# Performance work log

Measured on AMD Instinct MI355X. Metric: run time of the kernel, lower is better.

## Reference

```python
import jax, jax.numpy as jnp
import numpy as np

B = 2
SP = (480, 360, 32)   # spatial_shape (z, y, x)
GS = (8, 8, 8)        # query_gs_ratio
EP = (40, 15, 16)     # embed_params (pool compress ratio)
H = 8
N = 120000
D = 256
OUT = 20


def _dims(rat):
    return tuple((s + r - 1) // r for s, r in zip(SP, rat))


def sine_pe(coords, d_pos):
    # coords: [M,3] float voxel coords in original grid units; normalized sine PE
    nf = d_pos // 6
    sp = jnp.asarray(SP, jnp.float32)
    cn = coords / sp * (2.0 * jnp.pi)                      # normalize=True
    t = 10000.0 ** (jnp.arange(nf, dtype=jnp.float32) / nf)
    ang = cn[:, :, None] / t                               # [M,3,nf]
    pe = jnp.concatenate([jnp.sin(ang), jnp.cos(ang)], -1).reshape(coords.shape[0], -1)
    return jnp.pad(pe, ((0, 0), (0, d_pos - 6 * nf)))


def setup_inputs() -> dict:
    key = jax.random.key(0)
    ks = jax.random.split(key, 24)
    idx_b = jax.random.randint(ks[0], (N, 1), 0, B)
    idx_z = jax.random.randint(ks[1], (N, 1), 0, SP[0])
    idx_y = jax.random.randint(ks[2], (N, 1), 0, SP[1])
    idx_x = jax.random.randint(ks[3], (N, 1), 0, SP[2])
    indices = jnp.concatenate([idx_b, idx_z, idx_y, idx_x], axis=1).astype(jnp.int32)
    s = D ** -0.5
    p = lambda k, sh: jax.random.normal(k, sh, jnp.float32) * s
    return {
        'features': jax.random.normal(ks[4], (N, D), jnp.float32),
        'W_pool': p(ks[5], (D, D)), 'b_pool': jnp.zeros((D,), jnp.float32),
        'W_emb': p(ks[6], (D, D)), 'b_emb': jnp.zeros((D,), jnp.float32),
        'Wq': p(ks[7], (D, D)), 'bq': jnp.zeros((D,), jnp.float32),
        'Wk': p(ks[8], (D, D)), 'bk': jnp.zeros((D,), jnp.float32),
        'Wv': p(ks[9], (D, D)), 'bv': jnp.zeros((D,), jnp.float32),
        'Wo': p(ks[10], (D, D)), 'bo': jnp.zeros((D,), jnp.float32),
        'ln_g': jnp.ones((D,), jnp.float32), 'ln_b': jnp.zeros((D,), jnp.float32),
        'W_seg': p(ks[11], (D, OUT)), 'b_seg': jnp.zeros((OUT,), jnp.float32),
        'indices': indices,
        'batch_size': B,
    }


def reference(features, W_pool, b_pool, W_emb, b_emb, Wq, bq, Wk, bk, Wv, bv,
              Wo, bo, ln_g, ln_b, W_seg, b_seg, indices, batch_size):
    Zd, Yd, Xd = _dims(GS)
    Gq = Zd * Yd * Xd
    Sq = batch_size * Gq
    Ze, Ye, Xe = _dims(EP)
    Gk = Ze * Ye * Xe
    Sk = batch_size * Gk
    n = features.shape[0]

    # --- query pool branch: linear -> voxel-grid scatter_max ---
    pf = features @ W_pool + b_pool                                    # [N,D]
    dq = indices[:, 1:] // jnp.asarray(GS, jnp.int32)
    seg_q = ((indices[:, 0] * Zd + dq[:, 0]) * Yd + dq[:, 1]) * Xd + dq[:, 2]
    pool_max = jax.ops.segment_max(pf, seg_q, num_segments=Sq)
    cnt_q = jax.ops.segment_sum(jnp.ones((n,), jnp.float32), seg_q, num_segments=Sq)
    mq = cnt_q > 0
    pool_max = jnp.where(mq[:, None], pool_max, 0.0)
    cell = jnp.arange(Sq)
    rem = cell % Gq
    pool_c = jnp.stack([(rem // (Yd * Xd)) * GS[0],
                        ((rem // Xd) % Yd) * GS[1],
                        (rem % Xd) * GS[2]], -1).astype(jnp.float32)   # [Sq,3]

    # --- embedding branch ('pool'): linear -> coarse scatter_max + per-channel argmax coords ---
    ef = features @ W_emb + b_emb                                      # [N,D]
    de = indices[:, 1:] // jnp.asarray(EP, jnp.int32)
    seg_k = ((indices[:, 0] * Ze + de[:, 0]) * Ye + de[:, 1]) * Xe + de[:, 2]
    emb_max = jax.ops.segment_max(ef, seg_k, num_segments=Sk)
    cnt_k = jax.ops.segment_sum(jnp.ones((n,), jnp.float32), seg_k, num_segments=Sk)
    mk = cnt_k > 0
    emb_max = jnp.where(mk[:, None], emb_max, 0.0)
    winner = ef == jnp.where(mk[:, None], emb_max, -jnp.inf)[seg_k]
    idx = jax.ops.segment_max(jnp.where(winner, jnp.arange(n)[:, None], -1), seg_k, num_segments=Sk)
    idx_c = jnp.clip(idx, 0, n - 1)                                    # [Sk,D]
    ec = de.astype(jnp.float32)                                        # [N,3] downsampled coords
    emb_c = ec[idx_c].mean(axis=1) * jnp.asarray(EP, jnp.float32)      # [Sk,3]

    # --- position encoding (pointwise sine PE; per-batch loop in torch is pointwise-equivalent) ---
    pool_max = pool_max + sine_pe(pool_c, D)
    emb_max = emb_max + sine_pe(emb_c, D)

    # --- multi-head cross-attention (Q=pool, K/V=embedding), per-batch via dense grid reshape ---
    q_in = pool_max.reshape(batch_size, Gq, D)
    kv_in = emb_max.reshape(batch_size, Gk, D)
    dh = D // H
    q = (q_in @ Wq + bq).reshape(batch_size, Gq, H, dh)
    k = (kv_in @ Wk + bk).reshape(batch_size, Gk, H, dh)
    v = (kv_in @ Wv + bv).reshape(batch_size, Gk, H, dh)
    scores = jnp.einsum('bqhd,bkhd->bhqk', q, k) / jnp.float32(dh) ** 0.5
    kmask = mk.reshape(batch_size, Gk)
    scores = jnp.where(kmask[:, None, None, :], scores, -1e9)
    attn = jax.nn.softmax(scores, axis=-1)
    o = jnp.einsum('bhqk,bkhd->bqhd', attn, v).reshape(batch_size, Gq, D) @ Wo + bo
    h = q_in + o                                                       # residual + LayerNorm sublayer
    mu = h.mean(-1, keepdims=True)
    var = h.var(-1, keepdims=True)
    h = (h - mu) * jax.lax.rsqrt(var + 1e-5) * ln_g + ln_b
    feats_mhca = h.reshape(Sq, D)

    # --- gather back to voxels via pool_inv, residual, seg head (center-tap of SubMConv3d) ---
    vox = features + feats_mhca[seg_q]
    logits = vox @ W_seg + b_seg
    return logits
```

## Files before the change

kernel.cpp:

```cpp
#include <hip/hip_runtime.h>
#include <math.h>

#define N_PTS 120000
#define D 256
#define BATCH 2
#define NH 8
#define DH 32
#define OUTC 20

#define Zd 60
#define Yd 45
#define Xd 4
#define Gq 10800
#define Sq 21600

#define Ze 12
#define Ye 24
#define Xe 2
#define Gk 576
#define Sk 1152

typedef __bf16 bf16_t;
typedef __attribute__((ext_vector_type(8))) __bf16 bf16x8;
typedef __attribute__((ext_vector_type(4))) __bf16 bf16x4;
typedef __attribute__((ext_vector_type(4))) float f32x4;

__device__ __forceinline__ void glds16(const void* g, void* l) {
    __builtin_amdgcn_global_load_lds(
        (const __attribute__((address_space(1))) unsigned int*)g,
        (__attribute__((address_space(3))) unsigned int*)l,
        16, 0, 0);
}

__global__ __launch_bounds__(256) void k_prep(
    const float* __restrict__ Wp, const float* __restrict__ We,
    const float* __restrict__ Wq, const float* __restrict__ Wk,
    const float* __restrict__ Wv, const float* __restrict__ Wo,
    const float* __restrict__ bp, const float* __restrict__ be,
    const float* __restrict__ bk, const float* __restrict__ bv,
    const float* __restrict__ Wseg, const float* __restrict__ bseg,
    bf16_t* __restrict__ Wpe, bf16_t* __restrict__ Wqt,
    bf16_t* __restrict__ Wkv, bf16_t* __restrict__ Wot,
    bf16_t* __restrict__ Wsegt,
    float* __restrict__ bpe, float* __restrict__ bkv,
    float* __restrict__ bsegp)
{
    int n = blockIdx.x, k = threadIdx.x;
    if (n < 512) {
        const float* S = (n < 256) ? Wp : We;
        int nn = n & 255;
        Wpe[n * 256 + k] = (bf16_t)S[k * 256 + nn];
    } else if (n < 768) {
        int nn = n - 512;
        Wqt[nn * 256 + k] = (bf16_t)Wq[k * 256 + nn];
    } else if (n < 1280) {
        int m2 = n - 768;
        const float* S = (m2 < 256) ? Wk : Wv;
        int nn = m2 & 255;
        Wkv[m2 * 256 + k] = (bf16_t)S[k * 256 + nn];
    } else if (n < 1536) {
        int nn = n - 1280;
        Wot[nn * 256 + k] = (bf16_t)Wo[k * 256 + nn];
    } else if (n == 1536) {
        bpe[k] = bp[k]; bpe[256 + k] = be[k];
        bkv[k] = bk[k]; bkv[256 + k] = bv[k];
        if (k < 32) bsegp[k] = (k < OUTC) ? bseg[k] : 0.f;
    } else {
        int n2 = n - 1537;
        Wsegt[n2 * 256 + k] = (n2 < OUTC) ? (bf16_t)Wseg[k * OUTC + n2] : (bf16_t)0.f;
    }
}

__global__ __launch_bounds__(256) void k_cast(
    const float* __restrict__ in, bf16_t* __restrict__ out)
{
    const size_t total = (size_t)N_PTS * 32;
    const size_t stride = (size_t)gridDim.x * 256;
    for (size_t i = (size_t)blockIdx.x * 256 + threadIdx.x; i < total; i += stride) {
        float4 a = *(const float4*)(in + i * 8);
        float4 b = *(const float4*)(in + i * 8 + 4);
        bf16x8 o;
        o[0] = (bf16_t)a.x; o[1] = (bf16_t)a.y; o[2] = (bf16_t)a.z; o[3] = (bf16_t)a.w;
        o[4] = (bf16_t)b.x; o[5] = (bf16_t)b.y; o[6] = (bf16_t)b.z; o[7] = (bf16_t)b.w;
        *(bf16x8*)(out + i * 8) = o;
    }
}

__global__ __launch_bounds__(256) void k_count(
    const int* __restrict__ indices, int* __restrict__ cnt_q, int* __restrict__ cnt_k,
    int* __restrict__ segq, int* __restrict__ segk)
{
    int i = blockIdx.x * 256 + threadIdx.x;
    if (i >= N_PTS) return;
    const int* id = indices + (size_t)i * 4;
    int b = id[0], z = id[1], y = id[2], x = id[3];
    int sq = ((b * Zd + (z >> 3)) * Yd + (y >> 3)) * Xd + (x >> 3);
    int sk = ((b * Ze + (z / 40)) * Ye + (y / 15)) * Xe + (x >> 4);
    segq[i] = sq; segk[i] = sk;
    atomicAdd(&cnt_q[sq], 1);
    atomicAdd(&cnt_k[sk], 1);
}

__global__ __launch_bounds__(1024) void k_scan(
    const int* __restrict__ cnt, int n, int* __restrict__ offs, int* __restrict__ cursor)
{
    __shared__ int wbase[17];
    __shared__ int carry_s;
    const int t = threadIdx.x, lane = t & 63, w = t >> 6;
    if (t == 0) carry_s = 0;
    __syncthreads();
    for (int base = 0; base < n; base += 1024) {
        int v = (base + t < n) ? cnt[base + t] : 0;
        int incl = v;
        #pragma unroll
        for (int off = 1; off < 64; off <<= 1) {
            int u = __shfl_up(incl, off);
            if (lane >= off) incl += u;
        }
        if (lane == 63) wbase[w + 1] = incl;
        __syncthreads();
        if (t == 0) {
            int s = 0;
            wbase[0] = 0;
            #pragma unroll
            for (int i = 1; i <= 16; ++i) { s += wbase[i]; wbase[i] = s; }
        }
        __syncthreads();
        int excl = incl - v + wbase[w] + carry_s;
        if (base + t < n) { offs[base + t] = excl; cursor[base + t] = excl; }
        __syncthreads();
        if (t == 0) carry_s += wbase[16];
        __syncthreads();
    }
}

__global__ __launch_bounds__(256) void k_place(
    const int* __restrict__ segq, const int* __restrict__ segk,
    int* __restrict__ cur_q, int* __restrict__ cur_k,
    int* __restrict__ ids_q, int* __restrict__ ids_k)
{
    int i = blockIdx.x * 256 + threadIdx.x;
    if (i >= N_PTS) return;
    ids_q[atomicAdd(&cur_q[segq[i]], 1)] = i;
    ids_k[atomicAdd(&cur_k[segk[i]], 1)] = i;
}

__global__ __launch_bounds__(256, 4) void k_gemm_bf(
    const bf16_t* __restrict__ A, int M,
    const bf16_t* __restrict__ Wt, const float* __restrict__ bias,
    bf16_t* __restrict__ outb, int ldo)
{
    __shared__ __align__(16) bf16_t Abuf[128 * 64];
    __shared__ __align__(16) bf16_t Bbuf[128 * 64];

    const int t = threadIdx.x;
    const int wave = t >> 6, lane = t & 63;
    const int wr = wave >> 1, wc = wave & 1;
    const int lrow = lane & 15, quad = lane >> 4;
    const int lr8 = lane >> 3, lc8 = lane & 7;
    const int row0 = blockIdx.y * 128;
    const int ntile = blockIdx.x;

    f32x4 acc[4][4];
    #pragma unroll
    for (int mi = 0; mi < 4; ++mi)
        #pragma unroll
        for (int ni = 0; ni < 4; ++ni)
            acc[mi][ni] = (f32x4){0.f, 0.f, 0.f, 0.f};

    for (int k0 = 0; k0 < 256; k0 += 64) {
        #pragma unroll
        for (int i = 0; i < 4; ++i) {
            int chunk = wave * 4 + i;
            int rowA = row0 + chunk * 8 + lr8;
            if (rowA > M - 1) rowA = M - 1;
            glds16(A + (size_t)rowA * 256 + k0 + lc8 * 8, &Abuf[chunk * 512]);
        }
        #pragma unroll
        for (int i = 0; i < 4; ++i) {
            int chunk = wave * 4 + i;
            glds16(Wt + (size_t)(ntile * 128 + chunk * 8 + lr8) * 256 + k0 + lc8 * 8,
                   &Bbuf[chunk * 512]);
        }
        asm volatile("s_waitcnt vmcnt(0)" ::: "memory");
        __builtin_amdgcn_sched_barrier(0);
        __syncthreads();

        #pragma unroll
        for (int kk = 0; kk < 64; kk += 32) {
            bf16x8 Af[4], Bf[4];
            #pragma unroll
            for (int mi = 0; mi < 4; ++mi)
                Af[mi] = *(const bf16x8*)&Abuf[(wr * 64 + mi * 16 + lrow) * 64 + kk + quad * 8];
            #pragma unroll
            for (int ni = 0; ni < 4; ++ni)
                Bf[ni] = *(const bf16x8*)&Bbuf[(wc * 64 + ni * 16 + lrow) * 64 + kk + quad * 8];
            #pragma unroll
            for (int mi = 0; mi < 4; ++mi)
                #pragma unroll
                for (int ni = 0; ni < 4; ++ni)
                    acc[mi][ni] = __builtin_amdgcn_mfma_f32_16x16x32_bf16(
                        Af[mi], Bf[ni], acc[mi][ni], 0, 0, 0);
        }
        __syncthreads();
    }

    const int colb = ntile * 128 + wc * 64;
    float biasv[4];
    #pragma unroll
    for (int ni = 0; ni < 4; ++ni) biasv[ni] = bias[colb + ni * 16 + lrow];

    #pragma unroll
    for (int mi = 0; mi < 4; ++mi) {
        int lr = wr * 64 + mi * 16 + quad * 4;
        #pragma unroll
        for (int reg = 0; reg < 4; ++reg) {
            int grow = row0 + lr + reg;
            if (grow >= M) continue;
            #pragma unroll
            for (int ni = 0; ni < 4; ++ni) {
                int col = colb + ni * 16 + lrow;
                outb[(size_t)grow * ldo + col] = (bf16_t)(acc[mi][ni][reg] + biasv[ni]);
            }
        }
    }
}

__global__ __launch_bounds__(512, 2) void k_gemm(
    const float* __restrict__ A, int M,
    const bf16_t* __restrict__ Wt, const float* __restrict__ bias,
    int mode, float* __restrict__ outp, int ldo)
{
    __shared__ __align__(16) bf16_t Abuf[128][72];
    __shared__ __align__(16) bf16_t Bbuf[256][72];

    const int t = threadIdx.x;
    const int wave = t >> 6, lane = t & 63;
    const int wr = wave >> 2, wc = wave & 3;
    const int lrow = lane & 15, quad = lane >> 4;
    const int row0 = blockIdx.y * 128;
    const int ntile = blockIdx.x;

    f32x4 acc[4][4];
    #pragma unroll
    for (int mi = 0; mi < 4; ++mi)
        #pragma unroll
        for (int ni = 0; ni < 4; ++ni)
            acc[mi][ni] = (f32x4){0.f, 0.f, 0.f, 0.f};

    for (int k0 = 0; k0 < 256; k0 += 64) {
        #pragma unroll
        for (int i = 0; i < 4; ++i) {
            int c = i * 512 + t;
            int r = c >> 4, c4 = c & 15;
            float4 v = make_float4(0.f, 0.f, 0.f, 0.f);
            if (row0 + r < M)
                v = *(const float4*)(A + (size_t)(row0 + r) * 256 + k0 + c4 * 4);
            bf16x4 bv4;
            bv4[0] = (bf16_t)v.x; bv4[1] = (bf16_t)v.y;
            bv4[2] = (bf16_t)v.z; bv4[3] = (bf16_t)v.w;
            *(bf16x4*)&Abuf[r][c4 * 4] = bv4;
        }
        #pragma unroll
        for (int i = 0; i < 4; ++i) {
            int c = i * 512 + t;
            int r = c >> 3, c8 = c & 7;
            uint4 w = *(const uint4*)(Wt + ((size_t)(ntile * 256 + r)) * 256 + k0 + c8 * 8);
            *(uint4*)&Bbuf[r][c8 * 8] = w;
        }
        __syncthreads();

        #pragma unroll
        for (int kk = 0; kk < 64; kk += 32) {
            bf16x8 Af[4], Bf[4];
            #pragma unroll
            for (int mi = 0; mi < 4; ++mi)
                Af[mi] = *(const bf16x8*)&Abuf[wr * 64 + mi * 16 + lrow][kk + quad * 8];
            #pragma unroll
            for (int ni = 0; ni < 4; ++ni)
                Bf[ni] = *(const bf16x8*)&Bbuf[wc * 64 + ni * 16 + lrow][kk + quad * 8];
            #pragma unroll
            for (int mi = 0; mi < 4; ++mi)
                #pragma unroll
                for (int ni = 0; ni < 4; ++ni)
                    acc[mi][ni] = __builtin_amdgcn_mfma_f32_16x16x32_bf16(
                        Af[mi], Bf[ni], acc[mi][ni], 0, 0, 0);
        }
        __syncthreads();
    }

    const int colb = ntile * 256 + wc * 64;
    float biasv[4];
    #pragma unroll
    for (int ni = 0; ni < 4; ++ni) biasv[ni] = bias[colb + ni * 16 + lrow];

    if (mode == 0) {
        #pragma unroll
        for (int mi = 0; mi < 4; ++mi) {
            int lr = wr * 64 + mi * 16 + quad * 4;
            #pragma unroll
            for (int reg = 0; reg < 4; ++reg) {
                int grow = row0 + lr + reg;
                if (grow >= M) continue;
                #pragma unroll
                for (int ni = 0; ni < 4; ++ni) {
                    int col = colb + ni * 16 + lrow;
                    outp[(size_t)grow * ldo + col] = acc[mi][ni][reg] + biasv[ni];
                }
            }
        }
    } else {
        bf16_t* outb = (bf16_t*)outp;
        #pragma unroll
        for (int mi = 0; mi < 4; ++mi) {
            int lr = wr * 64 + mi * 16 + quad * 4;
            #pragma unroll
            for (int reg = 0; reg < 4; ++reg) {
                int grow = row0 + lr + reg;
                if (grow >= M) continue;
                #pragma unroll
                for (int ni = 0; ni < 4; ++ni) {
                    int col = colb + ni * 16 + lrow;
                    outb[(size_t)grow * ldo + col] = (bf16_t)(acc[mi][ni][reg] + biasv[ni]);
                }
            }
        }
    }
}

__device__ inline float pe_val(int j, float cz, float cy, float cx) {
    if (j >= 252) return 0.f;
    int dim = j / 84;
    int f = j % 84;
    int fi = (f >= 42) ? (f - 42) : f;
    float c  = (dim == 0) ? cz : ((dim == 1) ? cy : cx);
    float sp = (dim == 0) ? 480.f : ((dim == 1) ? 360.f : 32.f);
    float cn = c / sp * 6.28318530717958647692f;
    float tt = expf((float)fi * (9.210340371976184f / 42.f));
    float ang = cn / tt;
    return (f >= 42) ? cosf(ang) : sinf(ang);
}

__global__ __launch_bounds__(256) void k_pool_q(
    const bf16_t* __restrict__ pfb, const int* __restrict__ ids,
    const int* __restrict__ offs, const int* __restrict__ cnt,
    float* __restrict__ out)
{
    const int t = threadIdx.x, lane = t & 63, w = t >> 6;
    const int s = blockIdx.x * 4 + w;
    if (s >= Sq) return;
    const int count = cnt[s], start = offs[s];
    float mx[4] = {-3.0e38f, -3.0e38f, -3.0e38f, -3.0e38f};
    for (int r = 0; r < count; ++r) {
        int i = ids[start + r];
        bf16x4 v = *(const bf16x4*)(pfb + (size_t)i * 256 + lane * 4);
        #pragma unroll
        for (int j = 0; j < 4; ++j) mx[j] = fmaxf(mx[j], (float)v[j]);
    }
    int rem = s % Gq;
    float cz = (float)((rem / (Yd * Xd)) * 8);
    float cy = (float)(((rem / Xd) % Yd) * 8);
    float cx = (float)((rem % Xd) * 8);
    #pragma unroll
    for (int j = 0; j < 4; ++j) {
        float v = (count > 0) ? mx[j] : 0.f;
        out[(size_t)s * 256 + lane * 4 + j] = v + pe_val(lane * 4 + j, cz, cy, cx);
    }
}

__global__ __launch_bounds__(512) void k_pool_k(
    const bf16_t* __restrict__ efb, const int* __restrict__ ids,
    const int* __restrict__ offs, const int* __restrict__ cnt,
    float* __restrict__ out, int* __restrict__ kmask)
{
    __shared__ float red[8][256];
    const int t = threadIdx.x, lane = t & 63, w = t >> 6;
    const int s = blockIdx.x;
    const int count = cnt[s], start = offs[s];
    float mx[4] = {-3.0e38f, -3.0e38f, -3.0e38f, -3.0e38f};
    for (int r = w; r < count; r += 8) {
        int i = ids[start + r];
        bf16x4 v = *(const bf16x4*)(efb + (size_t)i * 256 + lane * 4);
        #pragma unroll
        for (int j = 0; j < 4; ++j) mx[j] = fmaxf(mx[j], (float)v[j]);
    }
    #pragma unroll
    for (int j = 0; j < 4; ++j) red[w][lane * 4 + j] = mx[j];
    __syncthreads();
    if (t < 256) {
        float m = red[0][t];
        #pragma unroll
        for (int i = 1; i < 8; ++i) m = fmaxf(m, red[i][t]);
        if (count == 0) m = 0.f;
        int rem = s % Gk;
        float cz = (float)((rem / (Ye * Xe)) * 40);
        float cy = (float)(((rem / Xe) % Ye) * 15);
        float cx = (float)((rem % Xe) * 16);
        out[(size_t)s * 256 + t] = m + pe_val(t, cz, cy, cx);
        if (t == 0) kmask[s] = (count > 0) ? 1 : 0;
    }
}

__global__ __launch_bounds__(256) void k_vt(
    const bf16_t* __restrict__ KVb, bf16_t* __restrict__ VT)
{
    int idx = blockIdx.x * 256 + threadIdx.x;
    if (idx >= 16 * 32 * 576) return;
    int g = idx % 576;
    int d = (idx / 576) & 31;
    int bh = idx / (576 * 32);
    int b = bh >> 3, h = bh & 7;
    VT[idx] = KVb[((size_t)(b * Gk + g)) * 512 + 256 + h * 32 + d];
}

__global__ __launch_bounds__(768, 3) void k_attn2(
    const bf16_t* __restrict__ Q, const bf16_t* __restrict__ KV,
    const bf16_t* __restrict__ VT, const int* __restrict__ kmask,
    float* __restrict__ O)
{
    __shared__ __align__(16) bf16_t Ks[576][40];
    __shared__ __align__(16) bf16_t Vts[32][584];
    __shared__ __align__(16) bf16_t Ps[12][16][104];
    __shared__ bf16_t mskb[576];

    const int bh = blockIdx.y;
    const int b = bh >> 3, h = bh & 7;
    const int t = threadIdx.x, wave = t >> 6, lane = t & 63;
    const int lrow = lane & 15, quad = lane >> 4;
    const int q0 = blockIdx.x * 192;

    #pragma unroll
    for (int i = 0; i < 3; ++i) {
        int id = i * 768 + t;
        int kk = id >> 2, part = id & 3;
        uint4 v = *(const uint4*)(KV + ((size_t)(b * Gk + kk)) * 512 + h * 32 + part * 8);
        *(uint4*)&Ks[kk][part * 8] = v;
    }
    #pragma unroll
    for (int i = 0; i < 3; ++i) {
        int id = i * 768 + t;
        int d = id / 72, c8 = id % 72;
        uint4 v = *(const uint4*)(VT + (size_t)(bh * 32 + d) * 576 + c8 * 8);
        *(uint4*)&Vts[d][c8 * 8] = v;
    }
    if (t < 576)
        mskb[t] = kmask[b * Gk + t] ? (bf16_t)0.f : (bf16_t)(-1.0e9f);
    __syncthreads();

    int qa = q0 + wave * 16 + lrow;
    if (qa > Gq - 1) qa = Gq - 1;
    const bf16x8 Aq = *(const bf16x8*)(Q + ((size_t)(b * Gq + qa)) * 256 + h * 32 + quad * 8);

    f32x4 oacc[2];
    oacc[0] = (f32x4){0.f, 0.f, 0.f, 0.f};
    oacc[1] = (f32x4){0.f, 0.f, 0.f, 0.f};
    float m_run[4], l_run[4];
    #pragma unroll
    for (int r = 0; r < 4; ++r) { m_run[r] = -3.0e38f; l_run[r] = 0.f; }

    for (int c0 = 0; c0 < Gk; c0 += 96) {
        float sreg[6][4];
        #pragma unroll
        for (int nt = 0; nt < 6; ++nt) {
            bf16x8 Bk = *(const bf16x8*)&Ks[c0 + nt * 16 + lrow][quad * 8];
            f32x4 sacc = __builtin_amdgcn_mfma_f32_16x16x32_bf16(
                Aq, Bk, (f32x4){0.f, 0.f, 0.f, 0.f}, 0, 0, 0);
            float pen = (float)mskb[c0 + nt * 16 + lrow];
            #pragma unroll
            for (int r = 0; r < 4; ++r)
                sreg[nt][r] = sacc[r] * 0.17677669529663688f + pen;
        }

        float alpha[4];
        #pragma unroll
        for (int r = 0; r < 4; ++r) {
            float mx = sreg[0][r];
            #pragma unroll
            for (int nt = 1; nt < 6; ++nt) mx = fmaxf(mx, sreg[nt][r]);
            #pragma unroll
            for (int off = 1; off < 16; off <<= 1)
                mx = fmaxf(mx, __shfl_xor(mx, off));
            float mnew = fmaxf(m_run[r], mx);
            alpha[r] = __expf(m_run[r] - mnew);
            m_run[r] = mnew;
            l_run[r] *= alpha[r];
        }
        #pragma unroll
        for (int n2 = 0; n2 < 2; ++n2)
            #pragma unroll
            for (int r = 0; r < 4; ++r) oacc[n2][r] *= alpha[r];

        float psum[4] = {0.f, 0.f, 0.f, 0.f};
        #pragma unroll
        for (int nt = 0; nt < 6; ++nt) {
            #pragma unroll
            for (int r = 0; r < 4; ++r) {
                float p = __expf(sreg[nt][r] - m_run[r]);
                psum[r] += p;
                Ps[wave][quad * 4 + r][nt * 16 + lrow] = (bf16_t)p;
            }
        }
        #pragma unroll
        for (int r = 0; r < 4; ++r) {
            float s = psum[r];
            #pragma unroll
            for (int off = 1; off < 16; off <<= 1) s += __shfl_xor(s, off);
            l_run[r] += s;
        }

        #pragma unroll
        for (int ks = 0; ks < 3; ++ks) {
            bf16x8 Ap = *(const bf16x8*)&Ps[wave][lrow][ks * 32 + quad * 8];
            #pragma unroll
            for (int n2 = 0; n2 < 2; ++n2) {
                bf16x8 Bv = *(const bf16x8*)&Vts[n2 * 16 + lrow][c0 + ks * 32 + quad * 8];
                oacc[n2] = __builtin_amdgcn_mfma_f32_16x16x32_bf16(
                    Ap, Bv, oacc[n2], 0, 0, 0);
            }
        }
    }

    #pragma unroll
    for (int r = 0; r < 4; ++r) {
        int qi = q0 + wave * 16 + quad * 4 + r;
        if (qi >= Gq) continue;
        float inv = (l_run[r] > 0.f) ? (1.f / l_run[r]) : 0.f;
        #pragma unroll
        for (int n2 = 0; n2 < 2; ++n2)
            O[((size_t)(b * Gq + qi)) * 256 + h * 32 + n2 * 16 + lrow] = oacc[n2][r] * inv;
    }
}

__global__ __launch_bounds__(256) void k_ln(
    const float* __restrict__ oproj, const float* __restrict__ resid,
    const float* __restrict__ g, const float* __restrict__ bta,
    float* __restrict__ out)
{
    const int s = blockIdx.x, t = threadIdx.x;
    float h = resid[(size_t)s * D + t] + oproj[(size_t)s * D + t];

    float s1 = h, s2 = h * h;
    for (int o = 32; o > 0; o >>= 1) {
        s1 += __shfl_down(s1, o);
        s2 += __shfl_down(s2, o);
    }
    __shared__ float r1[4], r2[4];
    __shared__ float mu_s, rstd_s;
    int w = t >> 6;
    if ((t & 63) == 0) { r1[w] = s1; r2[w] = s2; }
    __syncthreads();
    if (t == 0) {
        float a = r1[0] + r1[1] + r1[2] + r1[3];
        float bsum = r2[0] + r2[1] + r2[2] + r2[3];
        float mu = a * (1.f / 256.f);
        float var = bsum * (1.f / 256.f) - mu * mu;
        mu_s = mu;
        rstd_s = rsqrtf(var + 1e-5f);
    }
    __syncthreads();
    out[(size_t)s * D + t] = (h - mu_s) * rstd_s * g[t] + bta[t];
}

__global__ __launch_bounds__(512, 2) void k_logits_mfma(
    const float* __restrict__ feat, const float* __restrict__ mhca,
    const int* __restrict__ indices, const bf16_t* __restrict__ Wsegt,
    const float* __restrict__ bsegp, float* __restrict__ out)
{
    __shared__ __align__(16) bf16_t Abuf[128][72];
    __shared__ __align__(16) bf16_t Bbuf[32][72];
    __shared__ int sq_s[128];

    const int t = threadIdx.x;
    const int wave = t >> 6, lane = t & 63;
    const int lrow = lane & 15, quad = lane >> 4;
    const int row0 = blockIdx.x * 128;

    if (t < 128) {
        int row = row0 + t;
        if (row < N_PTS) {
            const int* id = indices + (size_t)row * 4;
            sq_s[t] = ((id[0] * Zd + (id[1] >> 3)) * Yd + (id[2] >> 3)) * Xd + (id[3] >> 3);
        } else sq_s[t] = 0;
    }
    __syncthreads();

    f32x4 acc[2];
    acc[0] = (f32x4){0.f, 0.f, 0.f, 0.f};
    acc[1] = (f32x4){0.f, 0.f, 0.f, 0.f};

    for (int k0 = 0; k0 < 256; k0 += 64) {
        #pragma unroll
        for (int i = 0; i < 4; ++i) {
            int c = i * 512 + t;
            int r = c >> 4, c4 = c & 15;
            float4 v = make_float4(0.f, 0.f, 0.f, 0.f);
            int grow = row0 + r;
            if (grow < N_PTS) {
                v = *(const float4*)(feat + (size_t)grow * 256 + k0 + c4 * 4);
                float4 m = *(const float4*)(mhca + (size_t)sq_s[r] * 256 + k0 + c4 * 4);
                v.x += m.x; v.y += m.y; v.z += m.z; v.w += m.w;
            }
            bf16x4 bv4;
            bv4[0] = (bf16_t)v.x; bv4[1] = (bf16_t)v.y;
            bv4[2] = (bf16_t)v.z; bv4[3] = (bf16_t)v.w;
            *(bf16x4*)&Abuf[r][c4 * 4] = bv4;
        }
        if (t < 256) {
            int r = t >> 3, c8 = t & 7;
            uint4 w = *(const uint4*)(Wsegt + (size_t)r * 256 + k0 + c8 * 8);
            *(uint4*)&Bbuf[r][c8 * 8] = w;
        }
        __syncthreads();

        #pragma unroll
        for (int kk = 0; kk < 64; kk += 32) {
            bf16x8 Af = *(const bf16x8*)&Abuf[wave * 16 + lrow][kk + quad * 8];
            #pragma unroll
            for (int ni = 0; ni < 2; ++ni) {
                bf16x8 Bf = *(const bf16x8*)&Bbuf[ni * 16 + lrow][kk + quad * 8];
                acc[ni] = __builtin_amdgcn_mfma_f32_16x16x32_bf16(
                    Af, Bf, acc[ni], 0, 0, 0);
            }
        }
        __syncthreads();
    }

    #pragma unroll
    for (int ni = 0; ni < 2; ++ni) {
        int col = ni * 16 + lrow;
        if (col >= OUTC) continue;
        float bias = bsegp[col];
        #pragma unroll
        for (int reg = 0; reg < 4; ++reg) {
            int grow = row0 + wave * 16 + quad * 4 + reg;
            if (grow >= N_PTS) continue;
            out[(size_t)grow * OUTC + col] = acc[ni][reg] + bias;
        }
    }
}

extern "C" void kernel_launch(void* const* d_in, const int* in_sizes, int n_in,
                              void* d_out, int out_size, void* d_ws, size_t ws_size,
                              hipStream_t stream) {
    const float* features = (const float*)d_in[0];
    const float* W_pool = (const float*)d_in[1];
    const float* b_pool = (const float*)d_in[2];
    const float* W_emb  = (const float*)d_in[3];
    const float* b_emb  = (const float*)d_in[4];
    const float* Wq = (const float*)d_in[5];
    const float* bq = (const float*)d_in[6];
    const float* Wk = (const float*)d_in[7];
    const float* bk = (const float*)d_in[8];
    const float* Wv = (const float*)d_in[9];
    const float* bv = (const float*)d_in[10];
    const float* Wo = (const float*)d_in[11];
    const float* bo = (const float*)d_in[12];
    const float* ln_g = (const float*)d_in[13];
    const float* ln_b = (const float*)d_in[14];
    const float* W_seg = (const float*)d_in[15];
    const float* b_seg = (const float*)d_in[16];
    const int* indices = (const int*)d_in[17];
    float* out = (float*)d_out;

    float* ws = (float*)d_ws;
    const size_t SQD = (size_t)Sq * D;
    const size_t SKD = (size_t)Sk * D;
    const size_t PFB_FL = (size_t)N_PTS * D / 2;

    size_t oP   = 0;
    size_t oPF  = oP + PFB_FL;
    size_t oEF  = oPF + SQD;
    size_t oWpe = oEF + SKD;
    size_t oWqt = oWpe + 65536;
    size_t oWkv = oWqt + 32768;
    size_t oWot = oWkv + 65536;
    size_t obpe = oWot + 32768;
    size_t obkv = obpe + 512;
    size_t oCnt = obkv + 512;
    size_t oOffq = oCnt + 21600 + 1152;
    size_t oCurq = oOffq + 21600;
    size_t oOffk = oCurq + 21600;
    size_t oCurk = oOffk + 1152;
    size_t oSegq = oCurk + 1152;
    size_t oSegk = oSegq + N_PTS;
    size_t oIdsq = oSegk + N_PTS;
    size_t oIdsk = oIdsq + N_PTS;
    size_t oKm   = oIdsk + N_PTS;
    size_t oWst  = oKm + 1152;
    size_t obsg  = oWst + 4096;
    size_t oFB   = obsg + 32;

    bf16_t* pfb = (bf16_t*)(ws + oP);
    float* pool_feat = ws + oPF;
    float* emb_feat  = ws + oEF;
    bf16_t* Wpe = (bf16_t*)(ws + oWpe);
    bf16_t* Wqt = (bf16_t*)(ws + oWqt);
    bf16_t* Wkv = (bf16_t*)(ws + oWkv);
    bf16_t* Wot = (bf16_t*)(ws + oWot);
    float* bpe = ws + obpe;
    float* bkv = ws + obkv;
    int* cnt_q = (int*)(ws + oCnt);
    int* cnt_k = cnt_q + 21600;
    int* offs_q = (int*)(ws + oOffq);
    int* cur_q  = (int*)(ws + oCurq);
    int* offs_k = (int*)(ws + oOffk);
    int* cur_k  = (int*)(ws + oCurk);
    int* segq = (int*)(ws + oSegq);
    int* segk = (int*)(ws + oSegk);
    int* ids_q = (int*)(ws + oIdsq);
    int* ids_k = (int*)(ws + oIdsk);
    int* kmask = (int*)(ws + oKm);
    bf16_t* Wsegt = (bf16_t*)(ws + oWst);
    float* bsegp = ws + obsg;
    bf16_t* fb16 = (bf16_t*)(ws + oFB);

    bf16_t* Qb  = (bf16_t*)(ws + oP);
    bf16_t* KVb = (bf16_t*)(ws + oP + 2764800);
    float* attnO = ws + oP + 3059712;
    float* oproj = ws + oP + 8589312;
    float* mhca  = ws + oP + 3059712;
    bf16_t* VT = (bf16_t*)(ws + oEF);

    const bool fast = ws_size >= (oFB + PFB_FL) * sizeof(float);

    hipMemsetAsync(cnt_q, 0, (21600 + 1152) * sizeof(int), stream);

    k_prep<<<1569, 256, 0, stream>>>(W_pool, W_emb, Wq, Wk, Wv, Wo,
                                     b_pool, b_emb, bk, bv, W_seg, b_seg,
                                     Wpe, Wqt, Wkv, Wot, Wsegt, bpe, bkv, bsegp);

    if (fast)
        k_cast<<<2048, 256, 0, stream>>>(features, fb16);

    k_count<<<(N_PTS + 255) / 256, 256, 0, stream>>>(indices, cnt_q, cnt_k, segq, segk);
    k_scan<<<1, 1024, 0, stream>>>(cnt_q, 21600, offs_q, cur_q);
    k_scan<<<1, 1024, 0, stream>>>(cnt_k, 1152, offs_k, cur_k);
    k_place<<<(N_PTS + 255) / 256, 256, 0, stream>>>(segq, segk, cur_q, cur_k, ids_q, ids_k);

    if (fast) {
        dim3 g(2, (N_PTS + 127) / 128);
        k_gemm_bf<<<g, 256, 0, stream>>>(fb16, N_PTS, Wpe + 256 * 256, bpe + 256,
                                         pfb, 256);
    } else {
        dim3 g(1, (N_PTS + 127) / 128);
        k_gemm<<<g, 512, 0, stream>>>(features, N_PTS, Wpe + 256 * 256, bpe + 256, 2,
                                      (float*)pfb, 256);
    }
    k_pool_k<<<Sk, 512, 0, stream>>>(pfb, ids_k, offs_k, cnt_k, emb_feat, kmask);

    if (fast) {
        dim3 g(2, (N_PTS + 127) / 128);
        k_gemm_bf<<<g, 256, 0, stream>>>(fb16, N_PTS, Wpe, bpe, pfb, 256);
    } else {
        dim3 g(1, (N_PTS + 127) / 128);
        k_gemm<<<g, 512, 0, stream>>>(features, N_PTS, Wpe, bpe, 2,
                                      (float*)pfb, 256);
    }
    k_pool_q<<<(Sq + 3) / 4, 256, 0, stream>>>(pfb, ids_q, offs_q, cnt_q, pool_feat);

    {
        dim3 g(1, (Sq + 127) / 128);
        k_gemm<<<g, 512, 0, stream>>>(pool_feat, Sq, Wqt, bq, 2, (float*)Qb, 256);
    }
    {
        dim3 g(2, (Sk + 127) / 128);
        k_gemm<<<g, 512, 0, stream>>>(emb_feat, Sk, Wkv, bkv, 2, (float*)KVb, 512);
    }

    k_vt<<<(16 * 32 * 576 + 255) / 256, 256, 0, stream>>>(KVb, VT);

    {
        dim3 ag((Gq + 191) / 192, BATCH * NH);
        k_attn2<<<ag, 768, 0, stream>>>(Qb, KVb, VT, kmask, attnO);
    }

    {
        dim3 g(1, (Sq + 127) / 128);
        k_gemm<<<g, 512, 0, stream>>>(attnO, Sq, Wot, bo, 0, oproj, 256);
    }

    k_ln<<<Sq, 256, 0, stream>>>(oproj, pool_feat, ln_g, ln_b, mhca);

    k_logits_mfma<<<(N_PTS + 127) / 128, 512, 0, stream>>>(
        features, mhca, indices, Wsegt, bsegp, out);
}
```

Before: 600.1 us.

## Fold attention scale into Q weights and read K from global in attention

New measurement: 599.8 us. About the same (-0.1%).

```diff
diff --git a/kernel.cpp b/kernel.cpp
--- a/kernel.cpp
+++ b/kernel.cpp
@@ -20,6 +20,8 @@
 #define Gk 576
 #define Sk 1152
 
+#define ATT_SCALE 0.17677669529663688f
+
 typedef __bf16 bf16_t;
 typedef __attribute__((ext_vector_type(8))) __bf16 bf16x8;
 typedef __attribute__((ext_vector_type(4))) __bf16 bf16x4;
@@ -37,13 +39,14 @@
     const float* __restrict__ Wq, const float* __restrict__ Wk,
     const float* __restrict__ Wv, const float* __restrict__ Wo,
     const float* __restrict__ bp, const float* __restrict__ be,
-    const float* __restrict__ bk, const float* __restrict__ bv,
+    const float* __restrict__ bq, const float* __restrict__ bk,
+    const float* __restrict__ bv,
     const float* __restrict__ Wseg, const float* __restrict__ bseg,
     bf16_t* __restrict__ Wpe, bf16_t* __restrict__ Wqt,
     bf16_t* __restrict__ Wkv, bf16_t* __restrict__ Wot,
     bf16_t* __restrict__ Wsegt,
     float* __restrict__ bpe, float* __restrict__ bkv,
-    float* __restrict__ bsegp)
+    float* __restrict__ bsegp, float* __restrict__ bqs)
 {
     int n = blockIdx.x, k = threadIdx.x;
     if (n < 512) {
@@ -52,7 +55,7 @@
         Wpe[n * 256 + k] = (bf16_t)S[k * 256 + nn];
     } else if (n < 768) {
         int nn = n - 512;
-        Wqt[nn * 256 + k] = (bf16_t)Wq[k * 256 + nn];
+        Wqt[nn * 256 + k] = (bf16_t)(Wq[k * 256 + nn] * ATT_SCALE);
     } else if (n < 1280) {
         int m2 = n - 768;
         const float* S = (m2 < 256) ? Wk : Wv;
@@ -64,6 +67,7 @@
     } else if (n == 1536) {
         bpe[k] = bp[k]; bpe[256 + k] = be[k];
         bkv[k] = bk[k]; bkv[256 + k] = bv[k];
+        bqs[k] = bq[k] * ATT_SCALE;
         if (k < 32) bsegp[k] = (k < OUTC) ? bseg[k] : 0.f;
     } else {
         int n2 = n - 1537;
@@ -413,15 +417,14 @@
     VT[idx] = KVb[((size_t)(b * Gk + g)) * 512 + 256 + h * 32 + d];
 }
 
-__global__ __launch_bounds__(768, 3) void k_attn2(
+__global__ __launch_bounds__(768, 6) void k_attn3(
     const bf16_t* __restrict__ Q, const bf16_t* __restrict__ KV,
     const bf16_t* __restrict__ VT, const int* __restrict__ kmask,
     float* __restrict__ O)
 {
-    __shared__ __align__(16) bf16_t Ks[576][40];
     __shared__ __align__(16) bf16_t Vts[32][584];
     __shared__ __align__(16) bf16_t Ps[12][16][104];
-    __shared__ bf16_t mskb[576];
+    __shared__ float mskf[576];
 
     const int bh = blockIdx.y;
     const int b = bh >> 3, h = bh & 7;
@@ -432,24 +435,19 @@
     #pragma unroll
     for (int i = 0; i < 3; ++i) {
         int id = i * 768 + t;
-        int kk = id >> 2, part = id & 3;
-        uint4 v = *(const uint4*)(KV + ((size_t)(b * Gk + kk)) * 512 + h * 32 + part * 8);
-        *(uint4*)&Ks[kk][part * 8] = v;
-    }
-    #pragma unroll
-    for (int i = 0; i < 3; ++i) {
-        int id = i * 768 + t;
         int d = id / 72, c8 = id % 72;
         uint4 v = *(const uint4*)(VT + (size_t)(bh * 32 + d) * 576 + c8 * 8);
         *(uint4*)&Vts[d][c8 * 8] = v;
     }
     if (t < 576)
-        mskb[t] = kmask[b * Gk + t] ? (bf16_t)0.f : (bf16_t)(-1.0e9f);
+        mskf[t] = kmask[b * Gk + t] ? 0.f : -1.0e9f;
     __syncthreads();
 
     int qa = q0 + wave * 16 + lrow;
     if (qa > Gq - 1) qa = Gq - 1;
     const bf16x8 Aq = *(const bf16x8*)(Q + ((size_t)(b * Gq + qa)) * 256 + h * 32 + quad * 8);
+
+    const bf16_t* Kbase = KV + ((size_t)b * Gk) * 512 + h * 32;
 
     f32x4 oacc[2];
     oacc[0] = (f32x4){0.f, 0.f, 0.f, 0.f};
@@ -462,13 +460,13 @@
         float sreg[6][4];
         #pragma unroll
         for (int nt = 0; nt < 6; ++nt) {
-            bf16x8 Bk = *(const bf16x8*)&Ks[c0 + nt * 16 + lrow][quad * 8];
+            bf16x8 Bk = *(const bf16x8*)(Kbase + (size_t)(c0 + nt * 16 + lrow) * 512 + quad * 8);
             f32x4 sacc = __builtin_amdgcn_mfma_f32_16x16x32_bf16(
                 Aq, Bk, (f32x4){0.f, 0.f, 0.f, 0.f}, 0, 0, 0);
-            float pen = (float)mskb[c0 + nt * 16 + lrow];
+            float pen = mskf[c0 + nt * 16 + lrow];
             #pragma unroll
             for (int r = 0; r < 4; ++r)
-                sreg[nt][r] = sacc[r] * 0.17677669529663688f + pen;
+                sreg[nt][r] = sacc[r] + pen;
         }
 
         float alpha[4];
@@ -688,7 +686,8 @@
     size_t oKm   = oIdsk + N_PTS;
     size_t oWst  = oKm + 1152;
     size_t obsg  = oWst + 4096;
-    size_t oFB   = obsg + 32;
+    size_t obqs  = obsg + 32;
+    size_t oFB   = obqs + 256;
 
     bf16_t* pfb = (bf16_t*)(ws + oP);
     float* pool_feat = ws + oPF;
@@ -712,6 +711,7 @@
     int* kmask = (int*)(ws + oKm);
     bf16_t* Wsegt = (bf16_t*)(ws + oWst);
     float* bsegp = ws + obsg;
+    float* bqs = ws + obqs;
     bf16_t* fb16 = (bf16_t*)(ws + oFB);
 
     bf16_t* Qb  = (bf16_t*)(ws + oP);
@@ -726,8 +726,8 @@
     hipMemsetAsync(cnt_q, 0, (21600 + 1152) * sizeof(int), stream);
 
     k_prep<<<1569, 256, 0, stream>>>(W_pool, W_emb, Wq, Wk, Wv, Wo,
-                                     b_pool, b_emb, bk, bv, W_seg, b_seg,
-                                     Wpe, Wqt, Wkv, Wot, Wsegt, bpe, bkv, bsegp);
+                                     b_pool, b_emb, bq, bk, bv, W_seg, b_seg,
+                                     Wpe, Wqt, Wkv, Wot, Wsegt, bpe, bkv, bsegp, bqs);
 
     if (fast)
         k_cast<<<2048, 256, 0, stream>>>(features, fb16);
@@ -760,7 +760,7 @@
 
     {
         dim3 g(1, (Sq + 127) / 128);
-        k_gemm<<<g, 512, 0, stream>>>(pool_feat, Sq, Wqt, bq, 2, (float*)Qb, 256);
+        k_gemm<<<g, 512, 0, stream>>>(pool_feat, Sq, Wqt, bqs, 2, (float*)Qb, 256);
     }
     {
         dim3 g(2, (Sk + 127) / 128);
@@ -771,7 +771,7 @@
 
     {
         dim3 ag((Gq + 191) / 192, BATCH * NH);
-        k_attn2<<<ag, 768, 0, stream>>>(Qb, KVb, VT, kmask, attnO);
+        k_attn3<<<ag, 768, 0, stream>>>(Qb, KVb, VT, kmask, attnO);
     }
 
     {
```
